# Performance work log

Hardware: AMD Instinct MI355X
Metric: run time of the kernel (lower is better)

The kernel has to match this reference:

```python
import jax, jax.numpy as jnp
import numpy as np

N_GROUPS = 32
EPS = 1e-6


def group_norm(x, gamma, beta):
    # x: (b, c, h, w); 32 groups, eps=1e-6, affine
    b, c, h, w = x.shape
    xg = x.reshape(b, N_GROUPS, c // N_GROUPS, h, w)
    mean = xg.mean(axis=(2, 3, 4), keepdims=True)
    var = xg.var(axis=(2, 3, 4), keepdims=True)
    xg = (xg - mean) * jax.lax.rsqrt(var + EPS)
    x = xg.reshape(b, c, h, w)
    return x * gamma[None, :, None, None] + beta[None, :, None, None]


def setup_inputs() -> dict:
    key = jax.random.key(0)
    ks = jax.random.split(key, 8)
    b, c, h, w = 4, 512, 64, 64
    sc = 1.0 / np.sqrt(c)
    return {
        "x": jax.random.normal(ks[0], (b, c, h, w), jnp.float32),
        "gn_w": jnp.ones((c,), jnp.float32),
        "gn_b": jnp.zeros((c,), jnp.float32),
        "wq": jax.random.normal(ks[1], (c, c), jnp.float32) * sc,
        "bq": jnp.zeros((c,), jnp.float32),
        "wk": jax.random.normal(ks[2], (c, c), jnp.float32) * sc,
        "bk": jnp.zeros((c,), jnp.float32),
        "wv": jax.random.normal(ks[3], (c, c), jnp.float32) * sc,
        "bv": jnp.zeros((c,), jnp.float32),
        "wo": jax.random.normal(ks[4], (c, c), jnp.float32) * sc,
        "bo": jnp.zeros((c,), jnp.float32),
    }


def reference(x, gn_w, gn_b, wq, bq, wk, bk, wv, bv, wo, bo):
    b, c, h, w = x.shape
    s = c ** (-0.5)
    xn = group_norm(x, gn_w, gn_b)
    xf = xn.reshape(b, c, h * w)  # (b, c, hw)
    # 1x1 convs == channel matmuls: weight (out_c, in_c)
    q = jnp.einsum('oc,bci->boi', wq, xf) + bq[None, :, None]
    k = jnp.einsum('oc,bci->boi', wk, xf) + bk[None, :, None]
    v = jnp.einsum('oc,bci->boi', wv, xf) + bv[None, :, None]
    attn = jnp.einsum('bci,bcj->bij', q, k) * s  # (b, hw, hw)
    attn = jax.nn.softmax(attn, axis=-1)
    out = jnp.einsum('bij,bcj->bci', attn, v)  # (b, c, hw)
    out = jnp.einsum('oc,bci->boi', wo, out) + bo[None, :, None]
    return out.reshape(b, c, h, w) + x
```

## Files before the change

kernel.cpp:

```cpp
#include <hip/hip_runtime.h>

#define B 4
#define C 512
#define HW 4096
#define NG 32
#define GSZ 65536

typedef unsigned short u16;
typedef unsigned int u32;
typedef __attribute__((ext_vector_type(8))) short short8;
typedef __attribute__((ext_vector_type(4))) float f32x4;

__device__ __forceinline__ float bf2f(u16 u) {
    union { u32 i; float f; } x; x.i = ((u32)u) << 16; return x.f;
}
__device__ __forceinline__ u16 f2bf(float f) {
    union { u32 i; float f; } x; x.f = f;
    u32 r = x.i + 0x7FFF + ((x.i >> 16) & 1);
    return (u16)(r >> 16);
}

__device__ __forceinline__ void gld16(const u16* g, u16* l) {
    __builtin_amdgcn_global_load_lds(
        (const __attribute__((address_space(1))) void*)g,
        (__attribute__((address_space(3))) void*)l, 16, 0, 0);
}

__global__ __launch_bounds__(256) void conv_kernel(
        const float* __restrict__ wq, const float* __restrict__ wk,
        const float* __restrict__ wv, const float* __restrict__ wo,
        u16* __restrict__ dst) {
    const int mat = blockIdx.y;
    const float* src = (mat == 0) ? wq : (mat == 1) ? wk : (mat == 2) ? wv : wo;
    const int idx = (blockIdx.x * 256 + threadIdx.x) * 4;
    float4 v = *(const float4*)(src + idx);
    ushort4 r;
    r.x = f2bf(v.x); r.y = f2bf(v.y); r.z = f2bf(v.z); r.w = f2bf(v.w);
    *(ushort4*)(dst + (size_t)mat * (C * C) + idx) = r;
}

__global__ __launch_bounds__(256) void gn_stats_kernel(
        const float* __restrict__ x, float2* __restrict__ part) {
    const int gl = blockIdx.x;
    const int qt = blockIdx.y;
    const size_t base = (size_t)gl * GSZ + (size_t)qt * (GSZ / 4);
    const int tid = threadIdx.x;
    float s = 0.f, s2 = 0.f;
    for (int i = tid * 4; i < GSZ / 4; i += 1024) {
        float4 v4 = *(const float4*)(x + base + i);
        s  += v4.x + v4.y + v4.z + v4.w;
        s2 += v4.x*v4.x + v4.y*v4.y + v4.z*v4.z + v4.w*v4.w;
    }
    #pragma unroll
    for (int off = 32; off > 0; off >>= 1) {
        s  += __shfl_down(s, off, 64);
        s2 += __shfl_down(s2, off, 64);
    }
    __shared__ float rs[4], rs2[4];
    int lane = tid & 63, wid = tid >> 6;
    if (lane == 0) { rs[wid] = s; rs2[wid] = s2; }
    __syncthreads();
    if (tid == 0) {
        part[gl * 4 + qt] = make_float2(rs[0] + rs[1] + rs[2] + rs[3],
                                        rs2[0] + rs2[1] + rs2[2] + rs2[3]);
    }
}

__global__ __launch_bounds__(256) void gn_apply_kernel(
        const float* __restrict__ x, const float* __restrict__ gamma,
        const float* __restrict__ beta, const float2* __restrict__ part,
        u16* __restrict__ xnT) {
    const int gl = blockIdx.y;
    const int b = gl >> 5, g = gl & 31;
    const size_t base = (size_t)gl * GSZ;
    const int i0 = blockIdx.x * 512;
    const int tid = threadIdx.x;
    float2 p0 = part[gl * 4 + 0], p1 = part[gl * 4 + 1];
    float2 p2 = part[gl * 4 + 2], p3 = part[gl * 4 + 3];
    float mean = (p0.x + p1.x + p2.x + p3.x) * (1.f / GSZ);
    float var  = (p0.y + p1.y + p2.y + p3.y) * (1.f / GSZ) - mean * mean;
    float rstd = rsqrtf(var + 1e-6f);
    const int c0 = g * 16;
    float gm[16], bt[16];
    #pragma unroll
    for (int c = 0; c < 16; c++) {
        float gg = gamma[c0 + c] * rstd;
        gm[c] = gg;
        bt[c] = beta[c0 + c] - mean * gg;
    }
    #pragma unroll 2
    for (int i = i0 + tid; i < i0 + 512; i += 256) {
        u32 pk[8];
        #pragma unroll
        for (int c = 0; c < 16; c += 2) {
            float a0 = x[base + (size_t)c * HW + i] * gm[c] + bt[c];
            float a1 = x[base + (size_t)(c + 1) * HW + i] * gm[c + 1] + bt[c + 1];
            pk[c >> 1] = (u32)f2bf(a0) | ((u32)f2bf(a1) << 16);
        }
        u16* dst = xnT + ((size_t)b * HW + i) * C + c0;
        *(uint4*)dst       = make_uint4(pk[0], pk[1], pk[2], pk[3]);
        *(uint4*)(dst + 8) = make_uint4(pk[4], pk[5], pk[6], pk[7]);
    }
}

__global__ __launch_bounds__(256) void qkv_kernel(
        const u16* __restrict__ xnT, const u16* __restrict__ wb,
        const float* __restrict__ bq, const float* __restrict__ bk,
        const float* __restrict__ bv,
        u16* __restrict__ qT, u16* __restrict__ kT, u16* __restrict__ vimg) {
    const int mat = blockIdx.y >> 2;
    const int oT0 = (blockIdx.y & 3) * 128;
    const int iT0 = blockIdx.x * 128;
    const int b = blockIdx.z;
    const u16* Ag = xnT + ((size_t)b * HW + iT0) * C;
    const u16* Bg = wb + (size_t)mat * C * C + (size_t)oT0 * C;
    const float* bias = (mat == 0) ? bq : (mat == 1) ? bk : bv;

    const int tid = threadIdx.x;
    const int w = tid >> 6, lane = tid & 63;
    const int qd = lane >> 4, nn = lane & 15;
    const int wm = w & 1, wn = w >> 1;

    __shared__ __align__(16) u16 As[2][128 * 32];
    __shared__ __align__(16) u16 Bs[2][128 * 32];

    f32x4 acc[4][4];
    #pragma unroll
    for (int mt = 0; mt < 4; mt++)
        #pragma unroll
        for (int nt = 0; nt < 4; nt++) acc[mt][nt] = (f32x4){0.f, 0.f, 0.f, 0.f};

    auto stage = [&](u16* dst, const u16* g, int c0) {
        #pragma unroll
        for (int p = 0; p < 2; p++) {
            int rbase = 32 * w + 16 * p;
            int row = rbase + (lane >> 2);
            gld16(g + (size_t)row * C + c0 + (((lane & 3) ^ ((row >> 1) & 3)) << 3),
                  dst + rbase * 32);
        }
    };

    stage(As[0], Ag, 0);
    stage(Bs[0], Bg, 0);

    for (int kt = 0; kt < 16; kt++) {
        const int cur = kt & 1;
        __syncthreads();
        if (kt < 15) {
            stage(As[cur ^ 1], Ag, (kt + 1) * 32);
            stage(Bs[cur ^ 1], Bg, (kt + 1) * 32);
        }
        short8 af[4], bf[4];
        #pragma unroll
        for (int mt = 0; mt < 4; mt++) {
            int row = 64 * wm + 16 * mt + nn;
            af[mt] = *(const short8*)&As[cur][row * 32 + ((qd ^ ((row >> 1) & 3)) << 3)];
        }
        #pragma unroll
        for (int nt = 0; nt < 4; nt++) {
            int row = 64 * wn + 16 * nt + nn;
            bf[nt] = *(const short8*)&Bs[cur][row * 32 + ((qd ^ ((row >> 1) & 3)) << 3)];
        }
        #pragma unroll
        for (int mt = 0; mt < 4; mt++)
            #pragma unroll
            for (int nt = 0; nt < 4; nt++)
                acc[mt][nt] = __builtin_amdgcn_mfma_f32_16x16x32_bf16(af[mt], bf[nt], acc[mt][nt], 0, 0, 0);
    }

    if (mat < 2) {
        u16* dstT = ((mat == 0) ? qT : kT) + (size_t)b * HW * C;
        #pragma unroll
        for (int nt = 0; nt < 4; nt++) {
            int o = oT0 + 64 * wn + 16 * nt + nn;
            float bb = bias[o];
            #pragma unroll
            for (int mt = 0; mt < 4; mt++) {
                int ib = iT0 + 64 * wm + 16 * mt + qd * 4;
                u16* p = dstT + (size_t)ib * C + o;
                p[0]     = f2bf(acc[mt][nt][0] + bb);
                p[C]     = f2bf(acc[mt][nt][1] + bb);
                p[2 * C] = f2bf(acc[mt][nt][2] + bb);
                p[3 * C] = f2bf(acc[mt][nt][3] + bb);
            }
        }
    } else {
        u16* vb = vimg + (size_t)b * 128 * 16384;
        #pragma unroll
        for (int nt = 0; nt < 4; nt++) {
            int c = oT0 + 64 * wn + 16 * nt + nn;
            float bb = bias[c];
            #pragma unroll
            for (int mt = 0; mt < 4; mt++) {
                int ib = iT0 + 64 * wm + 16 * mt + qd * 4;
                int ch = ib >> 5;
                int j0 = ib & 31;
                ushort4 st;
                st.x = f2bf(acc[mt][nt][0] + bb);
                st.y = f2bf(acc[mt][nt][1] + bb);
                st.z = f2bf(acc[mt][nt][2] + bb);
                st.w = f2bf(acc[mt][nt][3] + bb);
                *(ushort4*)&vb[(size_t)ch * 16384 + c * 32 +
                               (((j0 >> 3) ^ ((c >> 2) & 3)) << 3) + (j0 & 7)] = st;
            }
        }
    }
}

__global__ __launch_bounds__(256, 2) void attn_kernel(
        const u16* __restrict__ qT, const u16* __restrict__ kT,
        const u16* __restrict__ vimg, u16* __restrict__ oT) {
    const int b = blockIdx.y;
    const int i0 = blockIdx.x * 32;
    const int tid = threadIdx.x;
    const int w = tid >> 6;
    const int lane = tid & 63;
    const int q = lane >> 4;
    const int n = lane & 15;
    const int rw = w & 1;
    const int jh = w >> 1;

    __shared__ __align__(16) u16 kbuf[2][32 * 512];
    __shared__ __align__(16) u16 pbuf[2][32 * 40];
    __shared__ __align__(16) float mflag[2][4];
    __shared__ __align__(16) float lpart[2][32];

    short8 qf[16];
    {
        const u16* qrow = qT + ((size_t)b * HW + i0 + rw * 16 + n) * C + q * 8;
        #pragma unroll
        for (int k = 0; k < 16; k++) {
            uint4 u = *(const uint4*)(qrow + k * 32);
            qf[k] = *(const short8*)&u;
        }
    }
    f32x4 oacc[2][8];
    #pragma unroll
    for (int mt = 0; mt < 2; mt++)
        #pragma unroll
        for (int nt = 0; nt < 8; nt++)
            oacc[mt][nt] = (f32x4){0.f, 0.f, 0.f, 0.f};
    float mreg = 0.f;
    float lsum[4] = {0.f, 0.f, 0.f, 0.f};

    const u16* kTb = kT + (size_t)b * HW * C;
    const u16* vTb = vimg + (size_t)b * 128 * 16384;

    auto stageK = [&](int gc, int buf) {
        const u16* gk = kTb + (size_t)gc * 32 * C;
        #pragma unroll
        for (int ii = 0; ii < 8; ii++) {
            int j = w * 8 + ii;
            gld16(gk + (size_t)j * C + ((lane ^ (j & 7)) << 3), &kbuf[buf][j * 512]);
        }
    };

    const float scale = 0.04419417382415922f;
    stageK(0, 0);
    stageK(1, 1);
    __syncthreads();

    {
        f32x4 sa = {0.f,0.f,0.f,0.f}, sb = {0.f,0.f,0.f,0.f};
        const int sw = n & 7;
        const u16* kb = kbuf[0] + (jh * 16 + n) * 512;
        __builtin_amdgcn_s_setprio(1);
        #pragma unroll
        for (int kk = 0; kk < 8; kk++) {
            short8 bfa = *(const short8*)&kb[(((2 * kk) * 4 + q) ^ sw) << 3];
            short8 bfb = *(const short8*)&kb[(((2 * kk + 1) * 4 + q) ^ sw) << 3];
            sa = __builtin_amdgcn_mfma_f32_16x16x32_bf16(qf[2 * kk], bfa, sa, 0, 0, 0);
            sb = __builtin_amdgcn_mfma_f32_16x16x32_bf16(qf[2 * kk + 1], bfb, sb, 0, 0, 0);
        }
        __builtin_amdgcn_s_setprio(0);
        float sv[4];
        #pragma unroll
        for (int r = 0; r < 4; r++) sv[r] = (sa[r] + sb[r]) * scale;
        float pm = fmaxf(fmaxf(sv[0], sv[1]), fmaxf(sv[2], sv[3]));
        float flagv = -1e30f;
        if (__any(pm > mreg + 8.0f)) {
            float mx = pm;
            mx = fmaxf(mx, __shfl_xor(mx, 1));
            mx = fmaxf(mx, __shfl_xor(mx, 2));
            mx = fmaxf(mx, __shfl_xor(mx, 4));
            mx = fmaxf(mx, __shfl_xor(mx, 8));
            mx = fmaxf(mx, __shfl_xor(mx, 16));
            mx = fmaxf(mx, __shfl_xor(mx, 32));
            flagv = mx;
        }
        if (lane == 0) mflag[0][w] = flagv;
        #pragma unroll
        for (int r = 0; r < 4; r++) {
            float p = __expf(sv[r] - mreg);
            lsum[r] += p;
            pbuf[0][(rw * 16 + q * 4 + r) * 40 + jh * 16 + n] = f2bf(p);
        }
    }
    __syncthreads();

    #pragma unroll 1
    for (int t = 0; t < 128; ++t) {
        const int cur = t & 1;
        uint4 vpf[8];
        {
            const u16* gv = vTb + (size_t)t * 16384;
            #pragma unroll
            for (int nt = 0; nt < 8; nt++) {
                int c = w * 128 + nt * 16 + n;
                vpf[nt] = *(const uint4*)&gv[c * 32 + ((q ^ ((c >> 2) & 3)) << 3)];
            }
        }
        if (t < 126) stageK(t + 2, cur);
        f32x4 fl = *(const f32x4*)mflag[cur];
        float mnew = fmaxf(fmaxf(mreg, fl[0]), fmaxf(fmaxf(fl[1], fl[2]), fl[3]));
        float alpha = 1.f;
        if (mnew > mreg) { alpha = __expf(mreg - mnew); mreg = mnew; }
        if (t < 127) {
            f32x4 sa = {0.f,0.f,0.f,0.f}, sb = {0.f,0.f,0.f,0.f};
            const int sw = n & 7;
            const u16* kb = kbuf[cur ^ 1] + (jh * 16 + n) * 512;
            __builtin_amdgcn_s_setprio(1);
            #pragma unroll
            for (int kk = 0; kk < 8; kk++) {
                short8 bfa = *(const short8*)&kb[(((2 * kk) * 4 + q) ^ sw) << 3];
                short8 bfb = *(const short8*)&kb[(((2 * kk + 1) * 4 + q) ^ sw) << 3];
                sa = __builtin_amdgcn_mfma_f32_16x16x32_bf16(qf[2 * kk], bfa, sa, 0, 0, 0);
                sb = __builtin_amdgcn_mfma_f32_16x16x32_bf16(qf[2 * kk + 1], bfb, sb, 0, 0, 0);
            }
            __builtin_amdgcn_s_setprio(0);
            float sv[4];
            #pragma unroll
            for (int r = 0; r < 4; r++) sv[r] = (sa[r] + sb[r]) * scale;
            float pm = fmaxf(fmaxf(sv[0], sv[1]), fmaxf(sv[2], sv[3]));
            float flagv = -1e30f;
            if (__any(pm > mreg + 8.0f)) {
                float mx = pm;
                mx = fmaxf(mx, __shfl_xor(mx, 1));
                mx = fmaxf(mx, __shfl_xor(mx, 2));
                mx = fmaxf(mx, __shfl_xor(mx, 4));
                mx = fmaxf(mx, __shfl_xor(mx, 8));
                mx = fmaxf(mx, __shfl_xor(mx, 16));
                mx = fmaxf(mx, __shfl_xor(mx, 32));
                flagv = mx;
            }
            if (lane == 0) mflag[cur ^ 1][w] = flagv;
            #pragma unroll
            for (int r = 0; r < 4; r++) {
                float p = __expf(sv[r] - mreg);
                lsum[r] = lsum[r] * alpha + p;
                pbuf[cur ^ 1][(rw * 16 + q * 4 + r) * 40 + jh * 16 + n] = f2bf(p);
            }
        } else {
            #pragma unroll
            for (int r = 0; r < 4; r++) lsum[r] *= alpha;
        }
        short8 pf[2];
        #pragma unroll
        for (int mt = 0; mt < 2; mt++)
            pf[mt] = *(const short8*)&pbuf[cur][(mt * 16 + n) * 40 + q * 8];
        __builtin_amdgcn_s_setprio(1);
        #pragma unroll
        for (int nt = 0; nt < 8; nt++) {
            short8 vf = *(const short8*)&vpf[nt];
            #pragma unroll
            for (int mt = 0; mt < 2; mt++)
                oacc[mt][nt] = __builtin_amdgcn_mfma_f32_16x16x32_bf16(pf[mt], vf, oacc[mt][nt], 0, 0, 0);
        }
        __builtin_amdgcn_s_setprio(0);
        if (alpha != 1.f) {
            #pragma unroll
            for (int mt = 0; mt < 2; mt++)
                #pragma unroll
                for (int nt = 0; nt < 8; nt++) {
                    oacc[mt][nt][0] *= alpha; oacc[mt][nt][1] *= alpha;
                    oacc[mt][nt][2] *= alpha; oacc[mt][nt][3] *= alpha;
                }
        }
        __syncthreads();
    }
    #pragma unroll
    for (int r = 0; r < 4; r++) {
        float l = lsum[r];
        l += __shfl_xor(l, 1);
        l += __shfl_xor(l, 2);
        l += __shfl_xor(l, 4);
        l += __shfl_xor(l, 8);
        if (n == 0) lpart[jh][rw * 16 + q * 4 + r] = l;
    }
    __syncthreads();
    #pragma unroll
    for (int mt = 0; mt < 2; mt++) {
        float inv[4];
        #pragma unroll
        for (int r = 0; r < 4; r++) {
            int row = mt * 16 + q * 4 + r;
            inv[r] = 1.f / (lpart[0][row] + lpart[1][row]);
        }
        #pragma unroll
        for (int nt = 0; nt < 8; nt++) {
            int cc = w * 128 + nt * 16 + n;
            size_t base = ((size_t)b * HW + i0 + mt * 16 + q * 4) * C + cc;
            oT[base        ] = f2bf(oacc[mt][nt][0] * inv[0]);
            oT[base +   C  ] = f2bf(oacc[mt][nt][1] * inv[1]);
            oT[base + 2 * C] = f2bf(oacc[mt][nt][2] * inv[2]);
            oT[base + 3 * C] = f2bf(oacc[mt][nt][3] * inv[3]);
        }
    }
}

__global__ __launch_bounds__(256) void proj_kernel(
        const u16* __restrict__ oT, const u16* __restrict__ wob,
        const float* __restrict__ bo, const float* __restrict__ x,
        float* __restrict__ out) {
    const int o0 = blockIdx.y * 128;
    const int i0t = blockIdx.x * 128;
    const int b = blockIdx.z;
    const u16* Ag = wob + (size_t)o0 * C;
    const u16* Bg = oT + ((size_t)b * HW + i0t) * C;

    const int tid = threadIdx.x;
    const int w = tid >> 6, lane = tid & 63;
    const int qd = lane >> 4, nn = lane & 15;
    const int wm = w & 1, wn = w >> 1;

    __shared__ __align__(16) u16 As[2][128 * 32];
    __shared__ __align__(16) u16 Bs[2][128 * 32];

    f32x4 acc[4][4];
    #pragma unroll
    for (int mt = 0; mt < 4; mt++)
        #pragma unroll
        for (int nt = 0; nt < 4; nt++) acc[mt][nt] = (f32x4){0.f, 0.f, 0.f, 0.f};

    auto stage = [&](u16* dst, const u16* g, int c0) {
        #pragma unroll
        for (int p = 0; p < 2; p++) {
            int rbase = 32 * w + 16 * p;
            int row = rbase + (lane >> 2);
            gld16(g + (size_t)row * C + c0 + (((lane & 3) ^ ((row >> 1) & 3)) << 3),
                  dst + rbase * 32);
        }
    };

    stage(As[0], Ag, 0);
    stage(Bs[0], Bg, 0);

    for (int kt = 0; kt < 16; kt++) {
        const int cur = kt & 1;
        __syncthreads();
        if (kt < 15) {
            stage(As[cur ^ 1], Ag, (kt + 1) * 32);
            stage(Bs[cur ^ 1], Bg, (kt + 1) * 32);
        }
        short8 af[4], bf[4];
        #pragma unroll
        for (int mt = 0; mt < 4; mt++) {
            int row = 64 * wm + 16 * mt + nn;
            af[mt] = *(const short8*)&As[cur][row * 32 + ((qd ^ ((row >> 1) & 3)) << 3)];
        }
        #pragma unroll
        for (int nt = 0; nt < 4; nt++) {
            int row = 64 * wn + 16 * nt + nn;
            bf[nt] = *(const short8*)&Bs[cur][row * 32 + ((qd ^ ((row >> 1) & 3)) << 3)];
        }
        #pragma unroll
        for (int mt = 0; mt < 4; mt++)
            #pragma unroll
            for (int nt = 0; nt < 4; nt++)
                acc[mt][nt] = __builtin_amdgcn_mfma_f32_16x16x32_bf16(af[mt], bf[nt], acc[mt][nt], 0, 0, 0);
    }

    #pragma unroll
    for (int mt = 0; mt < 4; mt++) {
        #pragma unroll
        for (int r = 0; r < 4; r++) {
            int o = o0 + 64 * wm + 16 * mt + qd * 4 + r;
            float bb = bo[o];
            #pragma unroll
            for (int nt = 0; nt < 4; nt++) {
                int i = i0t + 64 * wn + 16 * nt + nn;
                size_t idx = ((size_t)b * C + o) * HW + i;
                out[idx] = acc[mt][nt][r] + bb + x[idx];
            }
        }
    }
}

extern "C" void kernel_launch(void* const* d_in, const int* in_sizes, int n_in,
                              void* d_out, int out_size, void* d_ws, size_t ws_size,
                              hipStream_t stream) {
    const float* x    = (const float*)d_in[0];
    const float* gn_w = (const float*)d_in[1];
    const float* gn_b = (const float*)d_in[2];
    const float* wq   = (const float*)d_in[3];
    const float* bq   = (const float*)d_in[4];
    const float* wk   = (const float*)d_in[5];
    const float* bk   = (const float*)d_in[6];
    const float* wv   = (const float*)d_in[7];
    const float* bv   = (const float*)d_in[8];
    const float* wo   = (const float*)d_in[9];
    const float* bo   = (const float*)d_in[10];
    float* out = (float*)d_out;

    const size_t WSZ = (size_t)C * C;
    const size_t S1  = (size_t)B * C * HW;
    u16* wb    = (u16*)d_ws;
    u16* wob   = wb + 3 * WSZ;
    u16* xnT   = wob + WSZ;
    u16* qT    = xnT + S1;
    u16* kT    = qT + S1;
    u16* vimg  = kT + S1;
    u16* oT    = vimg + S1;
    float2* part = (float2*)(oT + S1);

    hipLaunchKernelGGL(conv_kernel,     dim3(256, 4), dim3(256), 0, stream, wq, wk, wv, wo, wb);
    hipLaunchKernelGGL(gn_stats_kernel, dim3(B*NG, 4), dim3(256), 0, stream, x, part);
    hipLaunchKernelGGL(gn_apply_kernel, dim3(HW/512, B*NG), dim3(256), 0, stream,
                       x, gn_w, gn_b, part, xnT);
    hipLaunchKernelGGL(qkv_kernel,      dim3(HW/128, 12, B), dim3(256), 0, stream,
                       xnT, wb, bq, bk, bv, qT, kT, vimg);
    hipLaunchKernelGGL(attn_kernel,     dim3(HW/32, B), dim3(256), 0, stream,
                       qT, kT, vimg, oT);
    hipLaunchKernelGGL(proj_kernel,     dim3(HW/128, C/128, B), dim3(256), 0, stream, oT, wob, bo, x, out);
}
```

Before: 400.9 us.

## Pad K rows in LDS, use packed bf16 converts, split QK accumulators

Pads each K row in shared memory from 512 to 528 elements to change the LDS bank mapping of the QK^T fragment reads. Replaces the software round-to-nearest bf16 conversion with the v_cvt_pk_bf16_f32 instruction across the weight, groupnorm, V and P conversions. Splits the QK^T MFMA chain into four independent accumulators to shorten dependency latency. Hoists the P-fragment and max-flag LDS reads ahead of the V loads. Risks include more LDS and register use, which could cut occupancy, and tiny rounding differences from the hardware convert.

```diff
diff --git a/kernel.cpp b/kernel.cpp
--- a/kernel.cpp
+++ b/kernel.cpp
@@ -5,6 +5,7 @@
 #define HW 4096
 #define NG 32
 #define GSZ 65536
+#define KROW 528
 
 typedef unsigned short u16;
 typedef unsigned int u32;
@@ -18,6 +19,11 @@
     union { u32 i; float f; } x; x.f = f;
     u32 r = x.i + 0x7FFF + ((x.i >> 16) & 1);
     return (u16)(r >> 16);
+}
+__device__ __forceinline__ u32 cvtpk(float lo, float hi) {
+    u32 r;
+    asm("v_cvt_pk_bf16_f32 %0, %1, %2" : "=v"(r) : "v"(lo), "v"(hi));
+    return r;
 }
 
 __device__ __forceinline__ void gld16(const u16* g, u16* l) {
@@ -34,9 +40,8 @@
     const float* src = (mat == 0) ? wq : (mat == 1) ? wk : (mat == 2) ? wv : wo;
     const int idx = (blockIdx.x * 256 + threadIdx.x) * 4;
     float4 v = *(const float4*)(src + idx);
-    ushort4 r;
-    r.x = f2bf(v.x); r.y = f2bf(v.y); r.z = f2bf(v.z); r.w = f2bf(v.w);
-    *(ushort4*)(dst + (size_t)mat * (C * C) + idx) = r;
+    uint2 r = make_uint2(cvtpk(v.x, v.y), cvtpk(v.z, v.w));
+    *(uint2*)(dst + (size_t)mat * (C * C) + idx) = r;
 }
 
 __global__ __launch_bounds__(256) void gn_stats_kernel(
@@ -95,7 +100,7 @@
         for (int c = 0; c < 16; c += 2) {
             float a0 = x[base + (size_t)c * HW + i] * gm[c] + bt[c];
             float a1 = x[base + (size_t)(c + 1) * HW + i] * gm[c + 1] + bt[c + 1];
-            pk[c >> 1] = (u32)f2bf(a0) | ((u32)f2bf(a1) << 16);
+            pk[c >> 1] = cvtpk(a0, a1);
         }
         u16* dst = xnT + ((size_t)b * HW + i) * C + c0;
         *(uint4*)dst       = make_uint4(pk[0], pk[1], pk[2], pk[3]);
@@ -195,13 +200,11 @@
                 int ib = iT0 + 64 * wm + 16 * mt + qd * 4;
                 int ch = ib >> 5;
                 int j0 = ib & 31;
-                ushort4 st;
-                st.x = f2bf(acc[mt][nt][0] + bb);
-                st.y = f2bf(acc[mt][nt][1] + bb);
-                st.z = f2bf(acc[mt][nt][2] + bb);
-                st.w = f2bf(acc[mt][nt][3] + bb);
+                union { uint2 u; ushort4 s; } st;
+                st.u = make_uint2(cvtpk(acc[mt][nt][0] + bb, acc[mt][nt][1] + bb),
+                                  cvtpk(acc[mt][nt][2] + bb, acc[mt][nt][3] + bb));
                 *(ushort4*)&vb[(size_t)ch * 16384 + c * 32 +
-                               (((j0 >> 3) ^ ((c >> 2) & 3)) << 3) + (j0 & 7)] = st;
+                               (((j0 >> 3) ^ ((c >> 2) & 3)) << 3) + (j0 & 7)] = st.s;
             }
         }
     }
@@ -220,7 +223,7 @@
     const int rw = w & 1;
     const int jh = w >> 1;
 
-    __shared__ __align__(16) u16 kbuf[2][32 * 512];
+    __shared__ __align__(16) u16 kbuf[2][32 * KROW];
     __shared__ __align__(16) u16 pbuf[2][32 * 40];
     __shared__ __align__(16) float mflag[2][4];
     __shared__ __align__(16) float lpart[2][32];
@@ -251,7 +254,7 @@
         #pragma unroll
         for (int ii = 0; ii < 8; ii++) {
             int j = w * 8 + ii;
-            gld16(gk + (size_t)j * C + ((lane ^ (j & 7)) << 3), &kbuf[buf][j * 512]);
+            gld16(gk + (size_t)j * C + ((lane ^ (j & 7)) << 3), &kbuf[buf][j * KROW]);
         }
     };
 
@@ -260,22 +263,27 @@
     stageK(1, 1);
     __syncthreads();
 
-    {
-        f32x4 sa = {0.f,0.f,0.f,0.f}, sb = {0.f,0.f,0.f,0.f};
+    auto s_phase = [&](int slot, int par, float alpha) {
+        f32x4 s0 = {0.f,0.f,0.f,0.f}, s1 = {0.f,0.f,0.f,0.f};
+        f32x4 s2 = {0.f,0.f,0.f,0.f}, s3 = {0.f,0.f,0.f,0.f};
         const int sw = n & 7;
-        const u16* kb = kbuf[0] + (jh * 16 + n) * 512;
+        const u16* kb = kbuf[slot] + (jh * 16 + n) * KROW;
         __builtin_amdgcn_s_setprio(1);
         #pragma unroll
-        for (int kk = 0; kk < 8; kk++) {
-            short8 bfa = *(const short8*)&kb[(((2 * kk) * 4 + q) ^ sw) << 3];
-            short8 bfb = *(const short8*)&kb[(((2 * kk + 1) * 4 + q) ^ sw) << 3];
-            sa = __builtin_amdgcn_mfma_f32_16x16x32_bf16(qf[2 * kk], bfa, sa, 0, 0, 0);
-            sb = __builtin_amdgcn_mfma_f32_16x16x32_bf16(qf[2 * kk + 1], bfb, sb, 0, 0, 0);
+        for (int m = 0; m < 4; m++) {
+            short8 b0 = *(const short8*)&kb[(((4 * m + 0) * 4 + q) ^ sw) << 3];
+            short8 b1 = *(const short8*)&kb[(((4 * m + 1) * 4 + q) ^ sw) << 3];
+            short8 b2 = *(const short8*)&kb[(((4 * m + 2) * 4 + q) ^ sw) << 3];
+            short8 b3 = *(const short8*)&kb[(((4 * m + 3) * 4 + q) ^ sw) << 3];
+            s0 = __builtin_amdgcn_mfma_f32_16x16x32_bf16(qf[4 * m + 0], b0, s0, 0, 0, 0);
+            s1 = __builtin_amdgcn_mfma_f32_16x16x32_bf16(qf[4 * m + 1], b1, s1, 0, 0, 0);
+            s2 = __builtin_amdgcn_mfma_f32_16x16x32_bf16(qf[4 * m + 2], b2, s2, 0, 0, 0);
+            s3 = __builtin_amdgcn_mfma_f32_16x16x32_bf16(qf[4 * m + 3], b3, s3, 0, 0, 0);
         }
         __builtin_amdgcn_s_setprio(0);
         float sv[4];
         #pragma unroll
-        for (int r = 0; r < 4; r++) sv[r] = (sa[r] + sb[r]) * scale;
+        for (int r = 0; r < 4; r++) sv[r] = ((s0[r] + s1[r]) + (s2[r] + s3[r])) * scale;
         float pm = fmaxf(fmaxf(sv[0], sv[1]), fmaxf(sv[2], sv[3]));
         float flagv = -1e30f;
         if (__any(pm > mreg + 8.0f)) {
@@ -288,19 +296,32 @@
             mx = fmaxf(mx, __shfl_xor(mx, 32));
             flagv = mx;
         }
-        if (lane == 0) mflag[0][w] = flagv;
-        #pragma unroll
-        for (int r = 0; r < 4; r++) {
-            float p = __expf(sv[r] - mreg);
-            lsum[r] += p;
-            pbuf[0][(rw * 16 + q * 4 + r) * 40 + jh * 16 + n] = f2bf(p);
-        }
-    }
+        if (lane == 0) mflag[par][w] = flagv;
+        float p0 = __expf(sv[0] - mreg), p1 = __expf(sv[1] - mreg);
+        float p2 = __expf(sv[2] - mreg), p3 = __expf(sv[3] - mreg);
+        lsum[0] = lsum[0] * alpha + p0;
+        lsum[1] = lsum[1] * alpha + p1;
+        lsum[2] = lsum[2] * alpha + p2;
+        lsum[3] = lsum[3] * alpha + p3;
+        u32 a = cvtpk(p0, p1), c = cvtpk(p2, p3);
+        u16* pb = &pbuf[par][(rw * 16 + q * 4) * 40 + jh * 16 + n];
+        pb[0]      = (u16)a;
+        pb[40]     = (u16)(a >> 16);
+        pb[80]     = (u16)c;
+        pb[120]    = (u16)(c >> 16);
+    };
+
+    s_phase(0, 0, 1.f);
     __syncthreads();
 
     #pragma unroll 1
     for (int t = 0; t < 128; ++t) {
         const int cur = t & 1;
+        f32x4 fl = *(const f32x4*)mflag[cur];
+        short8 pf[2];
+        #pragma unroll
+        for (int mt = 0; mt < 2; mt++)
+            pf[mt] = *(const short8*)&pbuf[cur][(mt * 16 + n) * 40 + q * 8];
         uint4 vpf[8];
         {
             const u16* gv = vTb + (size_t)t * 16384;
@@ -311,53 +332,15 @@
             }
         }
         if (t < 126) stageK(t + 2, cur);
-        f32x4 fl = *(const f32x4*)mflag[cur];
         float mnew = fmaxf(fmaxf(mreg, fl[0]), fmaxf(fmaxf(fl[1], fl[2]), fl[3]));
         float alpha = 1.f;
         if (mnew > mreg) { alpha = __expf(mreg - mnew); mreg = mnew; }
         if (t < 127) {
-            f32x4 sa = {0.f,0.f,0.f,0.f}, sb = {0.f,0.f,0.f,0.f};
-            const int sw = n & 7;
-            const u16* kb = kbuf[cur ^ 1] + (jh * 16 + n) * 512;
-            __builtin_amdgcn_s_setprio(1);
-            #pragma unroll
-            for (int kk = 0; kk < 8; kk++) {
-                short8 bfa = *(const short8*)&kb[(((2 * kk) * 4 + q) ^ sw) << 3];
-                short8 bfb = *(const short8*)&kb[(((2 * kk + 1) * 4 + q) ^ sw) << 3];
-                sa = __builtin_amdgcn_mfma_f32_16x16x32_bf16(qf[2 * kk], bfa, sa, 0, 0, 0);
-                sb = __builtin_amdgcn_mfma_f32_16x16x32_bf16(qf[2 * kk + 1], bfb, sb, 0, 0, 0);
-            }
-            __builtin_amdgcn_s_setprio(0);
-            float sv[4];
-            #pragma unroll
-            for (int r = 0; r < 4; r++) sv[r] = (sa[r] + sb[r]) * scale;
-            float pm = fmaxf(fmaxf(sv[0], sv[1]), fmaxf(sv[2], sv[3]));
-            float flagv = -1e30f;
-            if (__any(pm > mreg + 8.0f)) {
-                float mx = pm;
-                mx = fmaxf(mx, __shfl_xor(mx, 1));
-                mx = fmaxf(mx, __shfl_xor(mx, 2));
-                mx = fmaxf(mx, __shfl_xor(mx, 4));
-                mx = fmaxf(mx, __shfl_xor(mx, 8));
-                mx = fmaxf(mx, __shfl_xor(mx, 16));
-                mx = fmaxf(mx, __shfl_xor(mx, 32));
-                flagv = mx;
-            }
-            if (lane == 0) mflag[cur ^ 1][w] = flagv;
-            #pragma unroll
-            for (int r = 0; r < 4; r++) {
-                float p = __expf(sv[r] - mreg);
-                lsum[r] = lsum[r] * alpha + p;
-                pbuf[cur ^ 1][(rw * 16 + q * 4 + r) * 40 + jh * 16 + n] = f2bf(p);
-            }
+            s_phase(cur ^ 1, cur ^ 1, alpha);
         } else {
             #pragma unroll
             for (int r = 0; r < 4; r++) lsum[r] *= alpha;
         }
-        short8 pf[2];
-        #pragma unroll
-        for (int mt = 0; mt < 2; mt++)
-            pf[mt] = *(const short8*)&pbuf[cur][(mt * 16 + n) * 40 + q * 8];
         __builtin_amdgcn_s_setprio(1);
         #pragma unroll
         for (int nt = 0; nt < 8; nt++) {
```

After: 383.7 us. 4.3% less time.
